# Performance work log

Measured on AMD Instinct MI355X. Metric: run time of the kernel, lower is better.

The kernel has to match this reference:

```python
import jax, jax.numpy as jnp
import numpy as np

D_MODEL = 1024
N_HEADS = 16
D_HEAD = 64  # = d_model // num_heads = d_inner
LN_EPS = 1e-5


def setup_inputs() -> dict:
    key = jax.random.key(0)
    ks = jax.random.split(key, 8)
    B, CUR, PREV = 2, 1024, 1024
    T = CUR + PREV
    s = 0.02
    return {
        "x": jax.random.normal(ks[0], (B, CUR, D_MODEL), jnp.float32),
        "pos_emb": jax.random.normal(ks[1], (T, D_MODEL), jnp.float32),
        "u": jax.random.normal(ks[2], (N_HEADS, D_HEAD), jnp.float32),
        "v": jax.random.normal(ks[3], (N_HEADS, D_HEAD), jnp.float32),
        "tgt_mask": jnp.ones((B, CUR, T, 1), jnp.bool_),
        "mem": jax.random.normal(ks[4], (B, PREV, D_MODEL), jnp.float32),
        "Wq": jax.random.normal(ks[5], (D_MODEL, D_MODEL), jnp.float32) * s,
        "Wkv": jax.random.normal(ks[6], (2 * D_MODEL, D_MODEL), jnp.float32) * s,
        "Wfc": jax.random.normal(ks[7], (D_MODEL, D_MODEL), jnp.float32) * s,
        "bfc": jnp.zeros((D_MODEL,), jnp.float32),
        "gamma": jnp.ones((D_MODEL,), jnp.float32),
        "beta": jnp.zeros((D_MODEL,), jnp.float32),
    }


def _rel_shift(x):
    # Faithful port of the torch _rel_shift: pad along the query axis (dim=1),
    # reinterpret the contiguous buffer as (I+1, B, J, H), drop first row, reshape back.
    B, I, J, H = x.shape
    zero_pad = jnp.zeros((B, 1, J, H), x.dtype)
    x_padded = jnp.concatenate([zero_pad, x], axis=1).reshape(I + 1, B, J, H)
    return x_padded[1:].reshape(B, I, J, H)


def reference(x, pos_emb, u, v, tgt_mask, mem, Wq, Wkv, Wfc, bfc, gamma, beta):
    B, CUR, _ = x.shape
    h = jnp.concatenate([mem, x], axis=1)          # (B, T, d_model)
    T = h.shape[1]
    q = (x @ Wq.T).reshape(B, CUR, N_HEADS, D_HEAD)
    kv = h @ Wkv.T                                  # (B, T, 2*d_model)
    k, vv = jnp.split(kv, 2, axis=-1)
    k = k.reshape(B, T, N_HEADS, D_HEAD)
    vv = vv.reshape(B, T, N_HEADS, D_HEAD)

    content_attn = jnp.einsum('bihd,bjhd->bijh', q + u, k)
    pe = pos_emb.reshape(T, N_HEADS, D_HEAD)
    pos_attn = _rel_shift(jnp.einsum('bihd,jhd->bijh', q + v, pe))

    attn = content_attn + pos_attn                  # (B, I, J, H)
    attn = jnp.where(tgt_mask == 0, -jnp.inf, attn)  # mask BEFORE scaling (as original)
    attn = attn / (D_HEAD ** 0.5)
    attn = jax.nn.softmax(attn, axis=1)             # NOTE: original softmaxes over dim=1 (query axis)

    weighted = jnp.einsum('bijh,bjhd->bihd', attn, vv).reshape(B, CUR, -1)
    y = x + weighted @ Wfc.T + bfc                  # residual + fc (post-norm path)
    mu = jnp.mean(y, axis=-1, keepdims=True)
    var = jnp.var(y, axis=-1, keepdims=True)
    return (y - mu) / jnp.sqrt(var + LN_EPS) * gamma + beta
```

## Files before the change

kernel.cpp:

```cpp
#include <hip/hip_runtime.h>

#define DM   1024
#define CUR  1024
#define TT   2048

typedef float  f32x4  __attribute__((ext_vector_type(4)));
typedef __bf16 bf16_t;
typedef __bf16 bf16x8 __attribute__((ext_vector_type(8)));
typedef __bf16 bf16x4 __attribute__((ext_vector_type(4)));
typedef short  s16x4  __attribute__((ext_vector_type(4)));

#define SCALE_A 0.18033688f

static __device__ __forceinline__ float exp2fast(float x) { return __builtin_amdgcn_exp2f(x); }
static __device__ __forceinline__ float log2fast(float x) { return __builtin_amdgcn_logf(x); }

static __device__ __forceinline__ f32x4 mfma32(bf16x8 a, bf16x8 b, f32x4 c) {
  return __builtin_amdgcn_mfma_f32_16x16x32_bf16(a, b, c, 0, 0, 0);
}
static __device__ __forceinline__ f32x4 mfma16(bf16x4 a, bf16x4 b, f32x4 c) {
  return __builtin_amdgcn_mfma_f32_16x16x16bf16_1k(
      __builtin_bit_cast(s16x4, a), __builtin_bit_cast(s16x4, b), c, 0, 0, 0);
}
static __device__ __forceinline__ void gl_lds16(const bf16_t* g, bf16_t* l) {
  __builtin_amdgcn_global_load_lds(
      (const __attribute__((address_space(1))) void*)g,
      (__attribute__((address_space(3))) void*)l, 16, 0, 0);
}

__global__ __launch_bounds__(256) void prep_kernel(const float* __restrict__ Wq,
                                                   const float* __restrict__ Wkv,
                                                   const float* __restrict__ Wfc,
                                                   const float* __restrict__ mem,
                                                   const float* __restrict__ x,
                                                   const float* __restrict__ pos,
                                                   bf16_t* __restrict__ wqb,
                                                   bf16_t* __restrict__ wkvb,
                                                   bf16_t* __restrict__ wfcb,
                                                   bf16_t* __restrict__ hb,
                                                   bf16_t* __restrict__ Bs) {
  int t = blockIdx.x * 256 + threadIdx.x;
  if (t < (1 << 20)) {
    const float* src; bf16_t* dst; int off;
    if (t < 262144)      { src = Wq;  dst = wqb;  off = t; }
    else if (t < 786432) { src = Wkv; dst = wkvb; off = t - 262144; }
    else                 { src = Wfc; dst = wfcb; off = t - 786432; }
    f32x4 v = *(const f32x4*)(src + (size_t)off * 4);
    bf16x4 o;
    o[0] = (bf16_t)v[0]; o[1] = (bf16_t)v[1]; o[2] = (bf16_t)v[2]; o[3] = (bf16_t)v[3];
    *(bf16x4*)(dst + (size_t)off * 4) = o;
  } else if (t < (2 << 20)) {
    int th = t - (1 << 20);
    int idx = th << 2;
    int b   = idx >> 21;
    int rem = idx & ((1 << 21) - 1);
    int tt  = rem >> 10;
    int c   = rem & 1023;
    const float* s = (tt < 1024)
        ? (mem + ((size_t)b * 1024 + tt) * DM + c)
        : (x   + ((size_t)b * 1024 + (tt - 1024)) * DM + c);
    f32x4 v = *(const f32x4*)s;
    bf16x4 o;
    o[0] = (bf16_t)v[0]; o[1] = (bf16_t)v[1]; o[2] = (bf16_t)v[2]; o[3] = (bf16_t)v[3];
    *(bf16x4*)(hb + idx) = o;
  } else {
    int tp = t - (2 << 20);
    int d4 = (tp & 15) << 2;
    int j  = (tp >> 4) & 2047;
    int bh = tp >> 15;
    int h  = bh & 15;
    f32x4 v = *(const f32x4*)(pos + (size_t)j * DM + h * 64 + d4);
    bf16x4 o;
    o[0] = (bf16_t)v[0]; o[1] = (bf16_t)v[1]; o[2] = (bf16_t)v[2]; o[3] = (bf16_t)v[3];
    *(bf16x4*)(Bs + ((size_t)bh * TT + j) * 128 + 64 + d4) = o;
  }
}

template<int WM>
__device__ __forceinline__ void gemm_core(const bf16_t* __restrict__ A,
                                          const bf16_t* __restrict__ B,
                                          int r0, int c0,
                                          bf16_t* At, bf16_t* Bt,
                                          f32x4 (&acc)[WM][4]) {
  const int ASZ = WM * 1024;
  const int BSZ = 4096;
  const int tid = threadIdx.x, w = tid >> 6, l = tid & 63;
  const int lm = l & 15, q = l >> 4;
  const int wrow = w >> 1, wcol = w & 1;
  const int gg  = (l & 3) ^ ((l >> 3) & 3);
  const int rsw = (lm >> 1) & 3;
  const bf16_t* gA = A + (size_t)(r0 + w * (WM / 2) * 16 + (l >> 2)) * 1024 + gg * 8;
  const bf16_t* gB = B + (size_t)(c0 + w * 32 + (l >> 2)) * 1024 + gg * 8;
  bf16_t* lA = At + w * (WM / 2) * 512;
  bf16_t* lB = Bt + w * 1024;
  const bf16_t* fA = At + (wrow * WM * 16 + lm) * 32;
  const bf16_t* fB = Bt + (wcol * 64 + lm) * 32;
#pragma unroll
  for (int t2 = 0; t2 < WM / 2; ++t2) gl_lds16(gA + (size_t)t2 * 16384, lA + t2 * 512);
#pragma unroll
  for (int t2 = 0; t2 < 2; ++t2)      gl_lds16(gB + (size_t)t2 * 16384, lB + t2 * 512);
  __syncthreads();
  int p = 0;
  for (int k0 = 0; k0 < 1024; k0 += 32) {
    int pn = p ^ 1;
    if (k0 < 992) {
#pragma unroll
      for (int t2 = 0; t2 < WM / 2; ++t2)
        gl_lds16(gA + (size_t)t2 * 16384 + k0 + 32, lA + pn * ASZ + t2 * 512);
#pragma unroll
      for (int t2 = 0; t2 < 2; ++t2)
        gl_lds16(gB + (size_t)t2 * 16384 + k0 + 32, lB + pn * BSZ + t2 * 512);
    }
    bf16x8 af[WM], bfm[4];
#pragma unroll
    for (int it = 0; it < WM; ++it)
      af[it] = *(const bf16x8*)(fA + p * ASZ + it * 512 + ((q ^ rsw) << 3));
#pragma unroll
    for (int jt = 0; jt < 4; ++jt)
      bfm[jt] = *(const bf16x8*)(fB + p * BSZ + jt * 512 + ((q ^ rsw) << 3));
#pragma unroll
    for (int it = 0; it < WM; ++it)
#pragma unroll
      for (int jt = 0; jt < 4; ++jt)
        acc[it][jt] = mfma32(af[it], bfm[jt], acc[it][jt]);
    __syncthreads();
    p = pn;
  }
}

__global__ __launch_bounds__(256) void k1_q(const bf16_t* __restrict__ hb,
                                            const bf16_t* __restrict__ Wqb,
                                            const float* __restrict__ u,
                                            const float* __restrict__ v,
                                            bf16_t* __restrict__ As) {
  __shared__ union { struct { bf16_t At[4096]; bf16_t Bt[8192]; } m; float Tt[4][272]; } sm;
  int blk = blockIdx.x;
  int r0 = (blk >> 3) * 64, c0 = (blk & 7) * 128;
  int b = r0 >> 10;
  const bf16_t* Axv = hb + ((size_t)(b + 1) << 20);
  f32x4 acc[2][4] = {};
  gemm_core<2>(Axv, Wqb, r0, c0, sm.m.At, sm.m.Bt, acc);
  const int tid = threadIdx.x, w = tid >> 6, l = tid & 63;
  const int lm = l & 15, q = l >> 4;
  const int wrow = w >> 1, wcol = w & 1;
  float* Tw = sm.Tt[w];
  int h = (c0 + wcol * 64) >> 6;
#pragma unroll
  for (int it = 0; it < 2; ++it) {
#pragma unroll
    for (int jt = 0; jt < 4; ++jt) {
#pragma unroll
      for (int r = 0; r < 4; ++r) Tw[(q * 4 + r) * 17 + lm] = acc[it][jt][r];
      __builtin_amdgcn_wave_barrier();
      int row = r0 + wrow * 32 + it * 16 + lm;
      int ii = row & 1023;
      int cbase = c0 + wcol * 64 + jt * 16 + q * 4;
      int d0 = cbase & 63;
      f32x4 u4 = *(const f32x4*)(u + cbase);
      f32x4 v4 = *(const f32x4*)(v + cbase);
      f32x4 tv;
#pragma unroll
      for (int e = 0; e < 4; ++e) tv[e] = Tw[lm * 17 + q * 4 + e];
      bf16x4 oc, op;
#pragma unroll
      for (int e = 0; e < 4; ++e) {
        oc[e] = (bf16_t)((tv[e] + u4[e]) * SCALE_A);
        op[e] = (bf16_t)((tv[e] + v4[e]) * SCALE_A);
      }
      *(bf16x4*)(As + (((size_t)(b * 16 + h)) * CUR + ii) * 128 + d0) = oc;
      if (b == 0) {
        if (ii >= 1)
          *(bf16x4*)(As + (((size_t)h) * CUR + (ii - 1)) * 128 + 64 + d0) = op;
        if (ii == 1023) {
          bf16x4 z = {};
          *(bf16x4*)(As + (((size_t)h) * CUR + 1023) * 128 + 64 + d0) = z;
        }
      } else {
        *(bf16x4*)(As + (((size_t)(16 + h)) * CUR + ii) * 128 + 64 + d0) = op;
      }
      __builtin_amdgcn_wave_barrier();
    }
  }
}

__global__ __launch_bounds__(256) void k2_kv(const bf16_t* __restrict__ hb,
                                             const bf16_t* __restrict__ Wkvb,
                                             bf16_t* __restrict__ Bs,
                                             bf16_t* __restrict__ vvT) {
  __shared__ union { struct { bf16_t At[8192]; bf16_t Bt[8192]; } m; float Tt[4][272]; } sm;
  int blk = blockIdx.x;
  int xcd = blk & 7, t = blk >> 3;
  int r0 = (t & 31) * 128;
  int c0 = (xcd * 2 + (t >> 5)) * 128;
  f32x4 acc[4][4] = {};
  gemm_core<4>(hb, Wkvb, r0, c0, sm.m.At, sm.m.Bt, acc);
  const int tid = threadIdx.x, w = tid >> 6, l = tid & 63;
  const int lm = l & 15, q = l >> 4;
  const int wrow = w >> 1, wcol = w & 1;
  int b = r0 >> 11;
  if (c0 < 1024) {
    float* Tw = sm.Tt[w];
    int h = (c0 + wcol * 64) >> 6;
#pragma unroll
    for (int it = 0; it < 4; ++it) {
#pragma unroll
      for (int jt = 0; jt < 4; ++jt) {
#pragma unroll
        for (int r = 0; r < 4; ++r) Tw[(q * 4 + r) * 17 + lm] = acc[it][jt][r];
        __builtin_amdgcn_wave_barrier();
        int j = (r0 + wrow * 64 + it * 16 + lm) & 2047;
        int d0 = jt * 16 + q * 4;
        bf16x4 o;
#pragma unroll
        for (int e = 0; e < 4; ++e) o[e] = (bf16_t)Tw[lm * 17 + q * 4 + e];
        *(bf16x4*)(Bs + (((size_t)(b * 16 + h)) * TT + j) * 128 + d0) = o;
        __builtin_amdgcn_wave_barrier();
      }
    }
  } else {
#pragma unroll
    for (int it = 0; it < 4; ++it) {
#pragma unroll
      for (int jt = 0; jt < 4; ++jt) {
        int c2 = c0 + wcol * 64 + jt * 16 + lm - 1024;
        int h = c2 >> 6, d = c2 & 63;
        int j = (r0 + wrow * 64 + it * 16 + q * 4) & 2047;
        bf16x4 o;
#pragma unroll
        for (int r = 0; r < 4; ++r) o[r] = (bf16_t)acc[it][jt][r];
        *(bf16x4*)(vvT + (((size_t)(b * 16 + h)) * 64 + d) * TT + j) = o;
      }
    }
  }
}

__global__ __launch_bounds__(256) void k3_stats(const bf16_t* __restrict__ As,
                                                const bf16_t* __restrict__ Bs,
                                                float* __restrict__ Lp) {
  __shared__ bf16_t At[2 * 8192];
  const int tid = threadIdx.x, w = tid >> 6, l = tid & 63;
  const int lm = l & 15, q = l >> 4;
  const int gg  = (l & 3) ^ ((l >> 3) & 3);
  const int rsw = (lm >> 1) & 3;
  int blk = blockIdx.x;
  int xcd = blk & 7, t = blk >> 3;
  int jblk = t & 15, ich = (t >> 4) & 1, bh = xcd * 4 + (t >> 5);
  int j0 = jblk * 128;
  const bf16_t* bsrow = Bs + ((size_t)bh * TT + j0 + w * 32 + lm) * 128 + q * 8;
  bf16x8 bfr[2][4];
#pragma unroll
  for (int js = 0; js < 2; ++js)
#pragma unroll
    for (int kt = 0; kt < 4; ++kt)
      bfr[js][kt] = *(const bf16x8*)(bsrow + js * 2048 + kt * 32);
  const bf16_t* abase = As + (size_t)bh * CUR * 128 +
                        (size_t)(ich * 512 + (l >> 2)) * 128 + w * 32 + gg * 8;
  bf16_t* lA = At + w * 2048;
  const bf16_t* fA = At + lm * 32;
  float l0 = 0.f, l1 = 0.f;
#pragma unroll
  for (int t2 = 0; t2 < 4; ++t2)
    gl_lds16(abase + (size_t)t2 * 16 * 128, lA + t2 * 512);
  __syncthreads();
  int p = 0;
  for (int ib = 0; ib < 8; ++ib) {
    int pn = p ^ 1;
    if (ib < 7) {
#pragma unroll
      for (int t2 = 0; t2 < 4; ++t2)
        gl_lds16(abase + (size_t)((ib + 1) * 64 + t2 * 16) * 128, lA + pn * 8192 + t2 * 512);
    }
#pragma unroll
    for (int isub = 0; isub < 4; ++isub) {
      bf16x8 af[4];
#pragma unroll
      for (int kt = 0; kt < 4; ++kt)
        af[kt] = *(const bf16x8*)(fA + p * 8192 + kt * 2048 + isub * 512 + ((q ^ rsw) << 3));
      f32x4 s0 = {}, s1 = {};
#pragma unroll
      for (int kt = 0; kt < 4; ++kt) {
        s0 = mfma32(af[kt], bfr[0][kt], s0);
        s1 = mfma32(af[kt], bfr[1][kt], s1);
      }
      l0 += exp2fast(s0[0]) + exp2fast(s0[1]) + exp2fast(s0[2]) + exp2fast(s0[3]);
      l1 += exp2fast(s1[0]) + exp2fast(s1[1]) + exp2fast(s1[2]) + exp2fast(s1[3]);
    }
    __syncthreads();
    p = pn;
  }
#pragma unroll
  for (int off = 16; off <= 32; off <<= 1) {
    l0 += __shfl_xor(l0, off, 64);
    l1 += __shfl_xor(l1, off, 64);
  }
  if (l < 16) {
    float* lp = Lp + (size_t)ich * 65536 + (size_t)bh * TT + j0 + w * 32;
    lp[l]      = l0;
    lp[16 + l] = l1;
  }
}

__global__ __launch_bounds__(256) void k3_comb(const float* __restrict__ Lp,
                                               float* __restrict__ LL) {
  int t = blockIdx.x * 256 + threadIdx.x;
  f32x4 a = *(const f32x4*)(Lp + (size_t)t * 4);
  f32x4 b = *(const f32x4*)(Lp + 65536 + (size_t)t * 4);
  f32x4 o;
#pragma unroll
  for (int e = 0; e < 4; ++e) o[e] = log2fast(a[e] + b[e]);
  *(f32x4*)(LL + (size_t)t * 4) = o;
}

__global__ __launch_bounds__(256) void k4_attnv(const bf16_t* __restrict__ As,
                                                const bf16_t* __restrict__ Bs,
                                                const bf16_t* __restrict__ vvT,
                                                const float* __restrict__ LL,
                                                float* __restrict__ Pp) {
  __shared__ union {
    struct { bf16_t Bt[2 * 8192]; bf16_t Vt[2 * 4096]; } m;
    float Tt[4][1088];
  } sm;
  int blk = blockIdx.x;
  int xcd = blk & 7, tb = blk >> 3;
  int iblk = tb & 7, pl = tb >> 3;
  int bh = xcd * 4 + (pl >> 2), jch = pl & 3;
  int b = bh >> 4, h = bh & 15;
  int i0 = iblk * 128;
  int jbase = jch * 512;
  const int tid = threadIdx.x, w = tid >> 6, l = tid & 63;
  const int lm = l & 15, q = l >> 4;
  const int gg  = (l & 3) ^ ((l >> 3) & 3);
  const int rsw = (lm >> 1) & 3;
  const bf16_t* ar = As + (size_t)bh * CUR * 128 + (size_t)(i0 + w * 32 + lm) * 128 + q * 8;
  bf16x8 bi[2][4];
#pragma unroll
  for (int is = 0; is < 2; ++is)
#pragma unroll
    for (int kt = 0; kt < 4; ++kt)
      bi[is][kt] = *(const bf16x8*)(ar + is * 2048 + kt * 32);
  const bf16_t* bbase = Bs + ((size_t)bh * TT + jbase) * 128 + (size_t)(l >> 2) * 128 + w * 32 + gg * 8;
  int inst0 = w * 2, inst1 = w * 2 + 1;
  const bf16_t* vsrc0 = vvT + ((size_t)bh * 64 + (inst0 & 3) * 16 + (l >> 2)) * TT + jbase +
                        (inst0 >> 2) * 32 + gg * 8;
  const bf16_t* vsrc1 = vvT + ((size_t)bh * 64 + (inst1 & 3) * 16 + (l >> 2)) * TT + jbase +
                        (inst1 >> 2) * 32 + gg * 8;
  bf16_t* vdst0 = sm.m.Vt + (inst0 >> 2) * 2048 + (inst0 & 3) * 512;
  bf16_t* vdst1 = sm.m.Vt + (inst1 >> 2) * 2048 + (inst1 & 3) * 512;
  bf16_t* lB = sm.m.Bt + w * 2048;
  const float* llb = LL + (size_t)bh * TT + jbase;
  f32x4 acc0[4] = {}, acc1[4] = {};
#pragma unroll
  for (int t2 = 0; t2 < 4; ++t2)
    gl_lds16(bbase + (size_t)t2 * 16 * 128, lB + t2 * 512);
  gl_lds16(vsrc0, vdst0);
  gl_lds16(vsrc1, vdst1);
  __syncthreads();
  int p = 0;
  for (int jb = 0; jb < 8; ++jb) {
    int pn = p ^ 1;
    if (jb < 7) {
      const bf16_t* bs2 = bbase + (size_t)(jb + 1) * 64 * 128;
#pragma unroll
      for (int t2 = 0; t2 < 4; ++t2)
        gl_lds16(bs2 + (size_t)t2 * 16 * 128, lB + pn * 8192 + t2 * 512);
      gl_lds16(vsrc0 + (jb + 1) * 64, vdst0 + pn * 4096);
      gl_lds16(vsrc1 + (jb + 1) * 64, vdst1 + pn * 4096);
    }
    const bf16_t* fB = sm.m.Bt + p * 8192 + lm * 32;
    const bf16_t* vf = sm.m.Vt + p * 4096 + lm * 32;
#pragma unroll
    for (int js = 0; js < 4; ++js) {
      bf16x8 af[4];
#pragma unroll
      for (int kt = 0; kt < 4; ++kt)
        af[kt] = *(const bf16x8*)(fB + kt * 2048 + js * 512 + ((q ^ rsw) << 3));
      f32x4 s0 = {}, s1 = {};
#pragma unroll
      for (int kt = 0; kt < 4; ++kt) {
        s0 = mfma32(af[kt], bi[0][kt], s0);
        s1 = mfma32(af[kt], bi[1][kt], s1);
      }
      f32x4 ll = *(const f32x4*)(llb + jb * 64 + js * 16 + q * 4);
      bf16x4 p0, p1;
#pragma unroll
      for (int e = 0; e < 4; ++e) {
        p0[e] = (bf16_t)exp2fast(s0[e] - ll[e]);
        p1[e] = (bf16_t)exp2fast(s1[e] - ll[e]);
      }
      int vg = ((js & 1) << 1) | (q >> 1);
      const bf16_t* vfa = vf + (js >> 1) * 2048 + ((vg ^ rsw) << 3) + ((q & 1) << 2);
#pragma unroll
      for (int dt = 0; dt < 4; ++dt) {
        bf16x4 a2 = *(const bf16x4*)(vfa + dt * 512);
        acc0[dt] = mfma16(a2, p0, acc0[dt]);
        acc1[dt] = mfma16(a2, p1, acc1[dt]);
      }
    }
    __syncthreads();
    p = pn;
  }
  float* Tw = sm.Tt[w];
  float* pout = Pp + ((size_t)jch << 21);
  int ir = l >> 2, dc = (l & 3) * 16;
#pragma unroll
  for (int is = 0; is < 2; ++is) {
#pragma unroll
    for (int dt = 0; dt < 4; ++dt) {
      f32x4 a = is ? acc1[dt] : acc0[dt];
#pragma unroll
      for (int r = 0; r < 4; ++r) Tw[(dt * 16 + q * 4 + r) * 17 + lm] = a[r];
    }
    __builtin_amdgcn_wave_barrier();
    int i = i0 + w * 32 + is * 16 + ir;
    float* orow = pout + ((size_t)(b * CUR + i)) * DM + h * 64 + dc;
#pragma unroll
    for (int e4 = 0; e4 < 4; ++e4) {
      f32x4 o;
#pragma unroll
      for (int e = 0; e < 4; ++e) o[e] = Tw[(dc + e4 * 4 + e) * 17 + ir];
      *(f32x4*)(orow + e4 * 4) = o;
    }
    __builtin_amdgcn_wave_barrier();
  }
}

__global__ __launch_bounds__(256) void k4_reduce(const float* __restrict__ P,
                                                 bf16_t* __restrict__ wbuf) {
  int t = blockIdx.x * 256 + threadIdx.x;
  f32x4 a = *(const f32x4*)(P + (size_t)t * 4);
  f32x4 b = *(const f32x4*)(P + (1u << 21) + (size_t)t * 4);
  f32x4 c = *(const f32x4*)(P + (2u << 21) + (size_t)t * 4);
  f32x4 d = *(const f32x4*)(P + (3u << 21) + (size_t)t * 4);
  bf16x4 o;
#pragma unroll
  for (int e = 0; e < 4; ++e) o[e] = (bf16_t)((a[e] + b[e]) + (c[e] + d[e]));
  *(bf16x4*)(wbuf + (size_t)t * 4) = o;
}

__global__ __launch_bounds__(256) void k5_fc(const bf16_t* __restrict__ wb,
                                             const bf16_t* __restrict__ Wfcb,
                                             const float* __restrict__ x,
                                             const float* __restrict__ bfc,
                                             float* __restrict__ y) {
  __shared__ union { struct { bf16_t At[4096]; bf16_t Bt[8192]; } m; float Tt[4][272]; } sm;
  int blk = blockIdx.x;
  int r0 = (blk >> 3) * 64, c0 = (blk & 7) * 128;
  f32x4 acc[2][4] = {};
  gemm_core<2>(wb, Wfcb, r0, c0, sm.m.At, sm.m.Bt, acc);
  const int tid = threadIdx.x, w = tid >> 6, l = tid & 63;
  const int lm = l & 15, q = l >> 4;
  const int wrow = w >> 1, wcol = w & 1;
  float* Tw = sm.Tt[w];
#pragma unroll
  for (int it = 0; it < 2; ++it) {
#pragma unroll
    for (int jt = 0; jt < 4; ++jt) {
#pragma unroll
      for (int r = 0; r < 4; ++r) Tw[(q * 4 + r) * 17 + lm] = acc[it][jt][r];
      __builtin_amdgcn_wave_barrier();
      int row = r0 + wrow * 32 + it * 16 + lm;
      int cb = c0 + wcol * 64 + jt * 16 + q * 4;
      f32x4 xb4 = *(const f32x4*)(x + (size_t)row * DM + cb);
      f32x4 bf4 = *(const f32x4*)(bfc + cb);
      f32x4 o;
#pragma unroll
      for (int e = 0; e < 4; ++e) o[e] = Tw[lm * 17 + q * 4 + e] + xb4[e] + bf4[e];
      *(f32x4*)(y + (size_t)row * DM + cb) = o;
      __builtin_amdgcn_wave_barrier();
    }
  }
}

__global__ __launch_bounds__(256) void k6_ln(const float* __restrict__ y,
                                             const float* __restrict__ gamma,
                                             const float* __restrict__ beta,
                                             float* __restrict__ out) {
  int row = blockIdx.x, t = threadIdx.x;
  const float* yr = y + (size_t)row * DM;
  f32x4 v = *(const f32x4*)(yr + t * 4);
  float s = v[0] + v[1] + v[2] + v[3];
  float ss = v[0] * v[0] + v[1] * v[1] + v[2] * v[2] + v[3] * v[3];
#pragma unroll
  for (int off = 1; off < 64; off <<= 1) {
    s += __shfl_xor(s, off, 64);
    ss += __shfl_xor(ss, off, 64);
  }
  __shared__ float ps[4], pss[4];
  int wv = t >> 6, ln = t & 63;
  if (ln == 0) { ps[wv] = s; pss[wv] = ss; }
  __syncthreads();
  s = ps[0] + ps[1] + ps[2] + ps[3];
  ss = pss[0] + pss[1] + pss[2] + pss[3];
  float mu = s * (1.0f / DM);
  float var = ss * (1.0f / DM) - mu * mu;
  float rstd = rsqrtf(var + 1e-5f);
  f32x4 g = *(const f32x4*)(gamma + t * 4);
  f32x4 bb = *(const f32x4*)(beta + t * 4);
  f32x4 o;
#pragma unroll
  for (int e = 0; e < 4; ++e) o[e] = (v[e] - mu) * rstd * g[e] + bb[e];
  *(f32x4*)(out + (size_t)row * DM + t * 4) = o;
}

extern "C" void kernel_launch(void* const* d_in, const int* in_sizes, int n_in,
                              void* d_out, int out_size, void* d_ws, size_t ws_size,
                              hipStream_t stream) {
  const float* x    = (const float*)d_in[0];
  const float* pos  = (const float*)d_in[1];
  const float* u    = (const float*)d_in[2];
  const float* v    = (const float*)d_in[3];
  const float* mem  = (const float*)d_in[5];
  const float* Wq   = (const float*)d_in[6];
  const float* Wkv  = (const float*)d_in[7];
  const float* Wfc  = (const float*)d_in[8];
  const float* bfc  = (const float*)d_in[9];
  const float* gam  = (const float*)d_in[10];
  const float* bet  = (const float*)d_in[11];
  float* out = (float*)d_out;

  char* ws = (char*)d_ws;
  const size_t MB = 1ull << 20;
  bf16_t* hb   = (bf16_t*)(ws);
  bf16_t* wqb  = (bf16_t*)(ws + 8 * MB);
  bf16_t* wkvb = (bf16_t*)(ws + 10 * MB);
  bf16_t* As   = (bf16_t*)(ws + 14 * MB);
  bf16_t* Bs   = (bf16_t*)(ws + 22 * MB);
  bf16_t* vvT  = (bf16_t*)(ws + 38 * MB);
  bf16_t* wfcb = (bf16_t*)(ws + 46 * MB);
  float*  LL   = (float*) (ws + 48 * MB);
  float*  Lp   = (float*) (ws + 48 * MB + 262144);
  float*  Pp   = (float*) (ws + 49 * MB);
  bf16_t* wbuf = (bf16_t*)(ws);
  float*  y    = (float*) (ws + 4 * MB);

  prep_kernel<<<12288, 256, 0, stream>>>(Wq, Wkv, Wfc, mem, x, pos,
                                         wqb, wkvb, wfcb, hb, Bs);
  k1_q<<<256, 256, 0, stream>>>(hb, wqb, u, v, As);
  k2_kv<<<512, 256, 0, stream>>>(hb, wkvb, Bs, vvT);

  k3_stats<<<1024, 256, 0, stream>>>(As, Bs, Lp);
  k3_comb<<<64, 256, 0, stream>>>(Lp, LL);
  k4_attnv<<<1024, 256, 0, stream>>>(As, Bs, vvT, LL, Pp);
  k4_reduce<<<2048, 256, 0, stream>>>(Pp, wbuf);

  k5_fc<<<256, 256, 0, stream>>>(wbuf, wfcb, x, bfc, y);
  k6_ln<<<2048, 256, 0, stream>>>(y, gam, bet, out);
}
```

Baseline: 246.6 us.

## Fold softmax normalizer into V and enlarge per-wave tiles in attention kernels

Softmax runs over the query axis, so the normalizer depends only on the key index. Instead of subtracting a per-key log-sum in the inner loop of the attention-V kernel, a new vscale kernel multiplies V in place by the reciprocal of the per-key sum, and the log-combine kernel is removed. Both the stats and attention-V kernels now give each wave 4 sub-tiles instead of 2, halving the grid and raising register use (launch bounds set to 2 waves per SIMD). The exp is computed without max-subtraction, so overflow safety relies on the value ranges, as it did before. Scaling V in bf16 adds an extra rounding step.

```diff
diff --git a/kernel.cpp b/kernel.cpp
--- a/kernel.cpp
+++ b/kernel.cpp
@@ -13,7 +13,6 @@
 #define SCALE_A 0.18033688f
 
 static __device__ __forceinline__ float exp2fast(float x) { return __builtin_amdgcn_exp2f(x); }
-static __device__ __forceinline__ float log2fast(float x) { return __builtin_amdgcn_logf(x); }
 
 static __device__ __forceinline__ f32x4 mfma32(bf16x8 a, bf16x8 b, f32x4 c) {
   return __builtin_amdgcn_mfma_f32_16x16x32_bf16(a, b, c, 0, 0, 0);
@@ -244,12 +243,12 @@
   const int rsw = (lm >> 1) & 3;
   int blk = blockIdx.x;
   int xcd = blk & 7, t = blk >> 3;
-  int jblk = t & 15, ich = (t >> 4) & 1, bh = xcd * 4 + (t >> 5);
-  int j0 = jblk * 128;
-  const bf16_t* bsrow = Bs + ((size_t)bh * TT + j0 + w * 32 + lm) * 128 + q * 8;
-  bf16x8 bfr[2][4];
-#pragma unroll
-  for (int js = 0; js < 2; ++js)
+  int jblk = t & 7, ich = (t >> 3) & 1, bh = xcd * 4 + (t >> 4);
+  int j0 = jblk * 256 + w * 64;
+  const bf16_t* bsrow = Bs + ((size_t)bh * TT + j0 + lm) * 128 + q * 8;
+  bf16x8 bfr[4][4];
+#pragma unroll
+  for (int js = 0; js < 4; ++js)
 #pragma unroll
     for (int kt = 0; kt < 4; ++kt)
       bfr[js][kt] = *(const bf16x8*)(bsrow + js * 2048 + kt * 32);
@@ -257,7 +256,7 @@
                         (size_t)(ich * 512 + (l >> 2)) * 128 + w * 32 + gg * 8;
   bf16_t* lA = At + w * 2048;
   const bf16_t* fA = At + lm * 32;
-  float l0 = 0.f, l1 = 0.f;
+  float lacc[4] = {0.f, 0.f, 0.f, 0.f};
 #pragma unroll
   for (int t2 = 0; t2 < 4; ++t2)
     gl_lds16(abase + (size_t)t2 * 16 * 128, lA + t2 * 512);
@@ -276,65 +275,79 @@
 #pragma unroll
       for (int kt = 0; kt < 4; ++kt)
         af[kt] = *(const bf16x8*)(fA + p * 8192 + kt * 2048 + isub * 512 + ((q ^ rsw) << 3));
-      f32x4 s0 = {}, s1 = {};
-#pragma unroll
-      for (int kt = 0; kt < 4; ++kt) {
-        s0 = mfma32(af[kt], bfr[0][kt], s0);
-        s1 = mfma32(af[kt], bfr[1][kt], s1);
-      }
-      l0 += exp2fast(s0[0]) + exp2fast(s0[1]) + exp2fast(s0[2]) + exp2fast(s0[3]);
-      l1 += exp2fast(s1[0]) + exp2fast(s1[1]) + exp2fast(s1[2]) + exp2fast(s1[3]);
+      f32x4 s[4] = {};
+#pragma unroll
+      for (int js = 0; js < 4; ++js)
+#pragma unroll
+        for (int kt = 0; kt < 4; ++kt)
+          s[js] = mfma32(af[kt], bfr[js][kt], s[js]);
+#pragma unroll
+      for (int js = 0; js < 4; ++js)
+        lacc[js] += (exp2fast(s[js][0]) + exp2fast(s[js][1])) +
+                    (exp2fast(s[js][2]) + exp2fast(s[js][3]));
     }
     __syncthreads();
     p = pn;
   }
 #pragma unroll
-  for (int off = 16; off <= 32; off <<= 1) {
-    l0 += __shfl_xor(l0, off, 64);
-    l1 += __shfl_xor(l1, off, 64);
+  for (int js = 0; js < 4; ++js) {
+#pragma unroll
+    for (int off = 16; off <= 32; off <<= 1)
+      lacc[js] += __shfl_xor(lacc[js], off, 64);
   }
   if (l < 16) {
-    float* lp = Lp + (size_t)ich * 65536 + (size_t)bh * TT + j0 + w * 32;
-    lp[l]      = l0;
-    lp[16 + l] = l1;
-  }
-}
-
-__global__ __launch_bounds__(256) void k3_comb(const float* __restrict__ Lp,
-                                               float* __restrict__ LL) {
-  int t = blockIdx.x * 256 + threadIdx.x;
-  f32x4 a = *(const f32x4*)(Lp + (size_t)t * 4);
-  f32x4 b = *(const f32x4*)(Lp + 65536 + (size_t)t * 4);
-  f32x4 o;
-#pragma unroll
-  for (int e = 0; e < 4; ++e) o[e] = log2fast(a[e] + b[e]);
-  *(f32x4*)(LL + (size_t)t * 4) = o;
-}
-
-__global__ __launch_bounds__(256) void k4_attnv(const bf16_t* __restrict__ As,
-                                                const bf16_t* __restrict__ Bs,
-                                                const bf16_t* __restrict__ vvT,
-                                                const float* __restrict__ LL,
-                                                float* __restrict__ Pp) {
+    float* lp = Lp + (size_t)ich * 65536 + (size_t)bh * TT + j0;
+#pragma unroll
+    for (int js = 0; js < 4; ++js) lp[js * 16 + l] = lacc[js];
+  }
+}
+
+__global__ __launch_bounds__(256) void vscale(const float* __restrict__ Lp,
+                                              bf16_t* __restrict__ vvT) {
+  int bh = blockIdx.x >> 3, jc = blockIdx.x & 7;
+  int tid = threadIdx.x;
+  int jj = jc * 256 + (tid & 63) * 4;
+  int dg = tid >> 6;
+  const float* lp = Lp + (size_t)bh * TT + jj;
+  f32x4 a = *(const f32x4*)lp;
+  f32x4 b = *(const f32x4*)(lp + 65536);
+  f32x4 rl;
+#pragma unroll
+  for (int e = 0; e < 4; ++e) rl[e] = __builtin_amdgcn_rcpf(a[e] + b[e]);
+  bf16_t* vb = vvT + ((size_t)bh * 64 + dg * 16) * TT + jj;
+#pragma unroll
+  for (int dd = 0; dd < 16; ++dd) {
+    bf16x4 vv = *(const bf16x4*)(vb + (size_t)dd * TT);
+    bf16x4 o;
+#pragma unroll
+    for (int e = 0; e < 4; ++e) o[e] = (bf16_t)((float)vv[e] * rl[e]);
+    *(bf16x4*)(vb + (size_t)dd * TT) = o;
+  }
+}
+
+__global__ __launch_bounds__(256, 2) void k4_attnv(const bf16_t* __restrict__ As,
+                                                   const bf16_t* __restrict__ Bs,
+                                                   const bf16_t* __restrict__ vvT,
+                                                   float* __restrict__ Pp) {
   __shared__ union {
     struct { bf16_t Bt[2 * 8192]; bf16_t Vt[2 * 4096]; } m;
     float Tt[4][1088];
   } sm;
   int blk = blockIdx.x;
   int xcd = blk & 7, tb = blk >> 3;
-  int iblk = tb & 7, pl = tb >> 3;
+  int iblk = tb & 3, pl = tb >> 2;
   int bh = xcd * 4 + (pl >> 2), jch = pl & 3;
   int b = bh >> 4, h = bh & 15;
-  int i0 = iblk * 128;
+  int i0 = iblk * 256;
   int jbase = jch * 512;
   const int tid = threadIdx.x, w = tid >> 6, l = tid & 63;
   const int lm = l & 15, q = l >> 4;
   const int gg  = (l & 3) ^ ((l >> 3) & 3);
   const int rsw = (lm >> 1) & 3;
-  const bf16_t* ar = As + (size_t)bh * CUR * 128 + (size_t)(i0 + w * 32 + lm) * 128 + q * 8;
-  bf16x8 bi[2][4];
-#pragma unroll
-  for (int is = 0; is < 2; ++is)
+  const bf16_t* ar = As + (size_t)bh * CUR * 128 + (size_t)(i0 + w * 64 + lm) * 128 + q * 8;
+  bf16x8 bi[4][4];
+#pragma unroll
+  for (int is = 0; is < 4; ++is)
 #pragma unroll
     for (int kt = 0; kt < 4; ++kt)
       bi[is][kt] = *(const bf16x8*)(ar + is * 2048 + kt * 32);
@@ -347,8 +360,7 @@
   bf16_t* vdst0 = sm.m.Vt + (inst0 >> 2) * 2048 + (inst0 & 3) * 512;
   bf16_t* vdst1 = sm.m.Vt + (inst1 >> 2) * 2048 + (inst1 & 3) * 512;
   bf16_t* lB = sm.m.Bt + w * 2048;
-  const float* llb = LL + (size_t)bh * TT + jbase;
-  f32x4 acc0[4] = {}, acc1[4] = {};
+  f32x4 acc[4][4] = {};
 #pragma unroll
   for (int t2 = 0; t2 < 4; ++t2)
     gl_lds16(bbase + (size_t)t2 * 16 * 128, lB + t2 * 512);
@@ -374,26 +386,26 @@
 #pragma unroll
       for (int kt = 0; kt < 4; ++kt)
         af[kt] = *(const bf16x8*)(fB + kt * 2048 + js * 512 + ((q ^ rsw) << 3));
-      f32x4 s0 = {}, s1 = {};
-#pragma unroll
-      for (int kt = 0; kt < 4; ++kt) {
-        s0 = mfma32(af[kt], bi[0][kt], s0);
-        s1 = mfma32(af[kt], bi[1][kt], s1);
-      }
-      f32x4 ll = *(const f32x4*)(llb + jb * 64 + js * 16 + q * 4);
-      bf16x4 p0, p1;
-#pragma unroll
-      for (int e = 0; e < 4; ++e) {
-        p0[e] = (bf16_t)exp2fast(s0[e] - ll[e]);
-        p1[e] = (bf16_t)exp2fast(s1[e] - ll[e]);
-      }
+      f32x4 s[4] = {};
+#pragma unroll
+      for (int is = 0; is < 4; ++is)
+#pragma unroll
+        for (int kt = 0; kt < 4; ++kt)
+          s[is] = mfma32(af[kt], bi[is][kt], s[is]);
+      bf16x4 pp[4];
+#pragma unroll
+      for (int is = 0; is < 4; ++is)
+#pragma unroll
+        for (int e = 0; e < 4; ++e)
+          pp[is][e] = (bf16_t)exp2fast(s[is][e]);
       int vg = ((js & 1) << 1) | (q >> 1);
       const bf16_t* vfa = vf + (js >> 1) * 2048 + ((vg ^ rsw) << 3) + ((q & 1) << 2);
 #pragma unroll
       for (int dt = 0; dt < 4; ++dt) {
         bf16x4 a2 = *(const bf16x4*)(vfa + dt * 512);
-        acc0[dt] = mfma16(a2, p0, acc0[dt]);
-        acc1[dt] = mfma16(a2, p1, acc1[dt]);
+#pragma unroll
+        for (int is = 0; is < 4; ++is)
+          acc[is][dt] = mfma16(a2, pp[is], acc[is][dt]);
       }
     }
     __syncthreads();
@@ -403,15 +415,15 @@
   float* pout = Pp + ((size_t)jch << 21);
   int ir = l >> 2, dc = (l & 3) * 16;
 #pragma unroll
-  for (int is = 0; is < 2; ++is) {
+  for (int is = 0; is < 4; ++is) {
 #pragma unroll
     for (int dt = 0; dt < 4; ++dt) {
-      f32x4 a = is ? acc1[dt] : acc0[dt];
+      f32x4 a = acc[is][dt];
 #pragma unroll
       for (int r = 0; r < 4; ++r) Tw[(dt * 16 + q * 4 + r) * 17 + lm] = a[r];
     }
     __builtin_amdgcn_wave_barrier();
-    int i = i0 + w * 32 + is * 16 + ir;
+    int i = i0 + w * 64 + is * 16 + ir;
     float* orow = pout + ((size_t)(b * CUR + i)) * DM + h * 64 + dc;
 #pragma unroll
     for (int e4 = 0; e4 < 4; ++e4) {
@@ -527,8 +539,7 @@
   bf16_t* Bs   = (bf16_t*)(ws + 22 * MB);
   bf16_t* vvT  = (bf16_t*)(ws + 38 * MB);
   bf16_t* wfcb = (bf16_t*)(ws + 46 * MB);
-  float*  LL   = (float*) (ws + 48 * MB);
-  float*  Lp   = (float*) (ws + 48 * MB + 262144);
+  float*  Lp   = (float*) (ws + 48 * MB);
   float*  Pp   = (float*) (ws + 49 * MB);
   bf16_t* wbuf = (bf16_t*)(ws);
   float*  y    = (float*) (ws + 4 * MB);
@@ -538,9 +549,9 @@
   k1_q<<<256, 256, 0, stream>>>(hb, wqb, u, v, As);
   k2_kv<<<512, 256, 0, stream>>>(hb, wkvb, Bs, vvT);
 
-  k3_stats<<<1024, 256, 0, stream>>>(As, Bs, Lp);
-  k3_comb<<<64, 256, 0, stream>>>(Lp, LL);
-  k4_attnv<<<1024, 256, 0, stream>>>(As, Bs, vvT, LL, Pp);
+  k3_stats<<<512, 256, 0, stream>>>(As, Bs, Lp);
+  vscale<<<256, 256, 0, stream>>>(Lp, vvT);
+  k4_attnv<<<512, 256, 0, stream>>>(As, Bs, vvT, Pp);
   k4_reduce<<<2048, 256, 0, stream>>>(Pp, wbuf);
 
   k5_fc<<<256, 256, 0, stream>>>(wbuf, wfcb, x, bfc, y);
```

After: 244.1 us. About the same (-1.0%).
